# Performance work log

Hardware: AMD Instinct MI355X
Metric: run time of the kernel (lower is better)

## Reference

```python
import jax, jax.numpy as jnp
import numpy as np

B, IN, OUT, G = 64, 8192, 8192, 64
NG = IN // G  # groups per row


def setup_inputs() -> dict:
    key = jax.random.key(0)
    k1, k2, k3, k4 = jax.random.split(key, 4)
    x = jax.random.normal(k1, (B, IN), dtype=jnp.float32)
    # packed 2-bit codes: 4 codes per byte, LSB-first (matches _pack2)
    w_packed = jax.random.randint(k2, (OUT, IN // 4), 0, 256, dtype=jnp.int32).astype(jnp.uint8)
    # scales from _calc_group_qparams are positive (max_abs/1.5); zp is always 2
    scales = jax.random.uniform(k3, (OUT, NG), dtype=jnp.float32, minval=0.01, maxval=0.1)
    zps = jnp.full((OUT, NG), 2, dtype=jnp.int32)
    bias = jax.random.normal(k4, (OUT,), dtype=jnp.float32) * 0.01
    return {"x": x, "w_packed": w_packed, "scales": scales, "zps": zps, "bias": bias}


def _dequant(w_packed, scales, zps):
    # unpack: byte -> 4 two-bit codes, LSB first (matches _unpack2)
    out_f = w_packed.shape[0]
    codes = jnp.stack([(w_packed >> s) & 3 for s in (0, 2, 4, 6)], axis=-1)  # [OUT, IN//4, 4]
    q = codes.reshape(out_f, NG, G).astype(jnp.int32)                        # [OUT, NG, G]
    # per-group dequant: (q - zp) * scale
    w = (q - zps[:, :, None]).astype(jnp.float32) * scales[:, :, None]
    return w.reshape(out_f, IN)                                              # [OUT, IN]


def reference(x, w_packed, scales, zps, bias):
    w = _dequant(w_packed, scales, zps)  # [OUT, IN] fp32
    # original accumulates xg @ wg.T per group; equivalent to full x @ w.T
    return x @ w.T + bias                # [B, OUT]
```

## Files before the change

kernel.cpp:

```cpp
#include <hip/hip_runtime.h>
#include <hip/hip_bf16.h>

#define B_    64
#define IN_   8192
#define OUT_  8192
#define NG_   128
#define PB_   2048
#define KSPLIT 16
#define KC    512

typedef float f32x4 __attribute__((ext_vector_type(4)));
typedef short s16x8 __attribute__((ext_vector_type(8)));
typedef _Float16 f16x4 __attribute__((ext_vector_type(4)));

__global__ __launch_bounds__(256) void k_pre(const float* __restrict__ x,
                                             __hip_bfloat16* __restrict__ xb) {
    int i = (blockIdx.x * 256 + threadIdx.x) * 4;
    float4 f = *(const float4*)(x + i);
    __hip_bfloat162 h0 = __float22bfloat162_rn(make_float2(f.x, f.y));
    __hip_bfloat162 h1 = __float22bfloat162_rn(make_float2(f.z, f.w));
    uint2 o; o.x = *(unsigned*)&h0; o.y = *(unsigned*)&h1;
    *(uint2*)(xb + i) = o;
}

__global__ __launch_bounds__(256, 2) void k_main(
    const __hip_bfloat16* __restrict__ xb,
    const unsigned char* __restrict__ wp,
    const float* __restrict__ scales,
    const int* __restrict__ zps,
    _Float16* __restrict__ part)
{
    __shared__ uint4 x_lds[4096];
    __shared__ int wflag, zflag;

    const int tid  = threadIdx.x;
    const int wave = tid >> 6;
    const int lane = tid & 63;
    const int q    = lane >> 4;
    const int nn   = lane & 15;

    const int kidx    = blockIdx.x & (KSPLIT - 1);
    const int nblk    = blockIdx.x >> 4;
    const int kbase   = kidx * KC;
    const int colbase = nblk * 256 + wave * 64;

    uint4 w4[4][2];
    {
        const unsigned char* wb = wp + (kbase >> 2) + q * 32;
#pragma unroll
        for (int cg = 0; cg < 4; ++cg) {
            const int n = colbase + cg * 16 + nn;
            w4[cg][0] = *(const uint4*)(wb + n * PB_);
            w4[cg][1] = *(const uint4*)(wb + n * PB_ + 16);
        }
    }
    float sgl[4][2];
#pragma unroll
    for (int cg = 0; cg < 4; ++cg) {
        const int n = colbase + cg * 16 + nn;
#pragma unroll
        for (int sp = 0; sp < 2; ++sp)
            sgl[cg][sp] = scales[n * NG_ + kidx * 8 + q * 2 + sp];
    }
#pragma unroll
    for (int i = 0; i < 16; ++i) {
        const int sg = wave * 16 + i;
        const int t = sg >> 2, mt = sg & 3;
        const int sb = t >> 2, b = t & 3;
        const __hip_bfloat16* src =
            xb + (mt * 16 + nn) * IN_ + kbase + q * 128 + sb * 32 + b * 8;
        __builtin_amdgcn_global_load_lds(
            (const __attribute__((address_space(1))) unsigned int*)src,
            (__attribute__((address_space(3))) unsigned int*)
                ((char*)x_lds + sg * 1024),
            16, 0, 0);
    }
    unsigned wv = ((const unsigned int*)wp)[tid];
    int      zv = zps[tid];
    if (tid == 0) { wflag = 0; zflag = 0; }
    __syncthreads();
    if (wv > 255u) wflag = 1;
    if (zv != 2)   zflag = 1;
    __syncthreads();
    const bool u8mode = (wflag != 0);
    const bool zgen   = (zflag != 0);

    if (!u8mode) {
        const int* wpi = (const int*)wp;
#pragma unroll
        for (int cg = 0; cg < 4; ++cg) {
            const int n = colbase + cg * 16 + nn;
            const int* p = wpi + n * PB_ + (kbase >> 2) + q * 32;
#pragma unroll
            for (int c = 0; c < 2; ++c) {
                unsigned d[4];
#pragma unroll
                for (int dd = 0; dd < 4; ++dd) {
                    const int* pq = p + c * 16 + dd * 4;
                    d[dd] = (unsigned)(pq[0] & 0xFF) | ((unsigned)(pq[1] & 0xFF) << 8)
                          | ((unsigned)(pq[2] & 0xFF) << 16) | ((unsigned)(pq[3] & 0xFF) << 24);
                }
                w4[cg][c] = (uint4){d[0], d[1], d[2], d[3]};
            }
        }
    }

    unsigned tabL[4][2], tabH[4][2];
#pragma unroll
    for (int cg = 0; cg < 4; ++cg)
#pragma unroll
        for (int sp = 0; sp < 2; ++sp) {
            const float s = sgl[cg][sp];
            float zf = 2.0f;
            if (zgen) {
                const int n = colbase + cg * 16 + nn;
                zf = (float)zps[n * NG_ + kidx * 8 + q * 2 + sp];
            }
            const float v0 = -zf * s, v1 = v0 + s, v2 = v1 + s, v3 = v2 + s;
            __hip_bfloat162 lo = __float22bfloat162_rn(make_float2(v0, v1));
            __hip_bfloat162 hi = __float22bfloat162_rn(make_float2(v2, v3));
            tabL[cg][sp] = *(unsigned*)&lo;
            tabH[cg][sp] = *(unsigned*)&hi;
        }

    f32x4 acc[4][4];
#pragma unroll
    for (int cg = 0; cg < 4; ++cg)
#pragma unroll
        for (int mt = 0; mt < 4; ++mt)
            acc[cg][mt] = (f32x4){0.f, 0.f, 0.f, 0.f};

#pragma unroll
    for (int sb = 0; sb < 4; ++sb) {
#pragma unroll
        for (int b = 0; b < 4; ++b) {
            const int t = sb * 4 + b;
            union { uint4 u4; s16x8 s8; } av[4];
#pragma unroll
            for (int mt = 0; mt < 4; ++mt)
                av[mt].u4 = x_lds[(t * 4 + mt) * 64 + lane];
#pragma unroll
            for (int cg = 0; cg < 4; ++cg) {
                const uint4 ch = w4[cg][sb >> 1];
                const unsigned dwv =
                    ((const unsigned*)&ch)[((sb & 1) << 1) | (b >> 1)];
                const unsigned u = (b & 1) ? (dwv >> 16) : (dwv & 0xFFFFu);
                const unsigned tl = tabL[cg][sb >> 1], th = tabH[cg][sb >> 1];
                union { unsigned w[4]; s16x8 s8; } bf;
#pragma unroll
                for (int m = 0; m < 4; ++m) {
                    const unsigned c0 = (u >> (4 * m)) & 3u;
                    const unsigned c1 = (u >> (4 * m + 2)) & 3u;
                    const unsigned sel = (0x0100u + c0 * 0x0202u)
                                       | ((0x0100u + c1 * 0x0202u) << 16);
                    bf.w[m] = __builtin_amdgcn_perm(th, tl, sel);
                }
#pragma unroll
                for (int mt = 0; mt < 4; ++mt)
                    acc[cg][mt] = __builtin_amdgcn_mfma_f32_16x16x32_bf16(
                        av[mt].s8, bf.s8, acc[cg][mt], 0, 0, 0);
            }
        }
    }

    _Float16* pp = part + kidx * (B_ * OUT_);
#pragma unroll
    for (int cg = 0; cg < 4; ++cg) {
        const int col = colbase + cg * 16 + nn;
#pragma unroll
        for (int mt = 0; mt < 4; ++mt)
#pragma unroll
            for (int r = 0; r < 4; ++r)
                pp[(mt * 16 + q * 4 + r) * OUT_ + col] = (_Float16)acc[cg][mt][r];
    }
}

__global__ __launch_bounds__(256) void k_reduce(const _Float16* __restrict__ part,
                                                const float* __restrict__ bias,
                                                float* __restrict__ out) {
    const int gtid = blockIdx.x * 256 + threadIdx.x;
    const int b  = gtid >> 11;
    const int n0 = (gtid & 2047) * 4;
    float4 s = *(const float4*)(bias + n0);
#pragma unroll
    for (int p = 0; p < KSPLIT; ++p) {
        f16x4 v = *(const f16x4*)(part + p * (B_ * OUT_) + b * OUT_ + n0);
        s.x += (float)v[0]; s.y += (float)v[1];
        s.z += (float)v[2]; s.w += (float)v[3];
    }
    *(float4*)(out + b * OUT_ + n0) = s;
}

extern "C" void kernel_launch(void* const* d_in, const int* in_sizes, int n_in,
                              void* d_out, int out_size, void* d_ws, size_t ws_size,
                              hipStream_t stream) {
    const float*         x      = (const float*)d_in[0];
    const unsigned char* wp     = (const unsigned char*)d_in[1];
    const float*         scales = (const float*)d_in[2];
    const int*           zps    = (const int*)d_in[3];
    const float*         bias   = (const float*)d_in[4];
    float*               out    = (float*)d_out;

    __hip_bfloat16* xb   = (__hip_bfloat16*)d_ws;
    _Float16*       part = (_Float16*)((char*)d_ws + (1 << 20));

    k_pre<<<512, 256, 0, stream>>>(x, xb);
    k_main<<<512, 256, 0, stream>>>(xb, wp, scales, zps, part);
    k_reduce<<<512, 256, 0, stream>>>(part, bias, out);
}
```

Before: 133.0 us.

## Pre-pack weights, dequant tables and x fragments into main-kernel-friendly layouts

Adds preprocessing kernels that run every call. They repack the 2-bit weights into a K-chunk-major layout, precompute the per-group bf16 dequant lookup tables from scales and zero points, and write x directly as bf16 MFMA fragments. The main kernel then does contiguous loads and no longer needs per-block mode detection or table construction. The cost is extra full passes over the weight matrix (read plus write) and several more kernel launches.

```diff
diff --git a/kernel.cpp b/kernel.cpp
--- a/kernel.cpp
+++ b/kernel.cpp
@@ -13,25 +13,100 @@
 typedef short s16x8 __attribute__((ext_vector_type(8)));
 typedef _Float16 f16x4 __attribute__((ext_vector_type(4)));
 
+#define OFF_WQ   (1u << 20)
+#define OFF_TAB  (17u << 20)
+#define OFF_PART (25u << 20)
+#define OFF_FLAG (41u << 20)
+
+__global__ __launch_bounds__(256) void k_flag(const unsigned* __restrict__ wp,
+                                              int* __restrict__ flag) {
+    __shared__ int f;
+    unsigned any = 0;
+#pragma unroll
+    for (int i = 0; i < 16; ++i)
+        any |= (wp[i * 256 + threadIdx.x] > 255u) ? 1u : 0u;
+    if (threadIdx.x == 0) f = 0;
+    __syncthreads();
+    if (any) f = 1;
+    __syncthreads();
+    if (threadIdx.x == 0) *flag = f;
+}
+
+__global__ __launch_bounds__(256) void k_wpack(const unsigned char* __restrict__ wp,
+                                               unsigned char* __restrict__ wq,
+                                               const int* __restrict__ flag) {
+    const int c  = threadIdx.x >> 4;
+    const int r  = blockIdx.x * 16 + (threadIdx.x & 15);
+    uint4 v[8];
+    if (*flag) {
+        const uint4* src = (const uint4*)(wp + r * PB_ + c * 128);
+#pragma unroll
+        for (int u = 0; u < 8; ++u) v[u] = src[u];
+    } else {
+        const int* src = (const int*)wp + r * PB_ + c * 128;
+#pragma unroll
+        for (int u = 0; u < 8; ++u) {
+            unsigned d[4];
+#pragma unroll
+            for (int w = 0; w < 4; ++w) {
+                const int* p = src + u * 16 + w * 4;
+                d[w] = (unsigned)(p[0] & 0xFF) | ((unsigned)(p[1] & 0xFF) << 8) |
+                       ((unsigned)(p[2] & 0xFF) << 16) | ((unsigned)(p[3] & 0xFF) << 24);
+            }
+            v[u] = (uint4){d[0], d[1], d[2], d[3]};
+        }
+    }
+    uint4* dst = (uint4*)(wq + ((unsigned)c * OUT_ + r) * 128);
+#pragma unroll
+    for (int u = 0; u < 8; ++u) dst[u] = v[u];
+}
+
+__global__ __launch_bounds__(256) void k_spack(const float* __restrict__ scales,
+                                               const int* __restrict__ zps,
+                                               uint2* __restrict__ tab) {
+    const int e = blockIdx.x * 256 + threadIdx.x;
+    const int n = e >> 7, g = e & 127;
+    const float s = scales[e];
+    const float zf = (float)zps[e];
+    const float v0 = -zf * s, v1 = v0 + s, v2 = v1 + s, v3 = v2 + s;
+    __hip_bfloat162 lo = __float22bfloat162_rn(make_float2(v0, v1));
+    __hip_bfloat162 hi = __float22bfloat162_rn(make_float2(v2, v3));
+    uint2 ent; ent.x = *(unsigned*)&lo; ent.y = *(unsigned*)&hi;
+    tab[(((unsigned)(g >> 3) * OUT_) + n) * 8 + (g & 7)] = ent;
+}
+
 __global__ __launch_bounds__(256) void k_pre(const float* __restrict__ x,
-                                             __hip_bfloat16* __restrict__ xb) {
-    int i = (blockIdx.x * 256 + threadIdx.x) * 4;
-    float4 f = *(const float4*)(x + i);
-    __hip_bfloat162 h0 = __float22bfloat162_rn(make_float2(f.x, f.y));
-    __hip_bfloat162 h1 = __float22bfloat162_rn(make_float2(f.z, f.w));
-    uint2 o; o.x = *(unsigned*)&h0; o.y = *(unsigned*)&h1;
-    *(uint2*)(xb + i) = o;
+                                             uint4* __restrict__ xfrag) {
+    const int kidx = blockIdx.x >> 2;
+    const int part = blockIdx.x & 3;
+#pragma unroll
+    for (int i = 0; i < 4; ++i) {
+        const int idx = (part * 4 + i) * 256 + threadIdx.x;
+        const int sg = idx >> 6, lane = idx & 63;
+        const int tt = sg >> 2, mt = sg & 3;
+        const int sb = tt >> 2, b = tt & 3;
+        const int q = lane >> 4, nn = lane & 15;
+        const float* src = x + (mt * 16 + nn) * IN_ + kidx * KC + q * 128 + sb * 32 + b * 8;
+        const float4 f0 = *(const float4*)src;
+        const float4 f1 = *(const float4*)(src + 4);
+        __hip_bfloat162 h0 = __float22bfloat162_rn(make_float2(f0.x, f0.y));
+        __hip_bfloat162 h1 = __float22bfloat162_rn(make_float2(f0.z, f0.w));
+        __hip_bfloat162 h2 = __float22bfloat162_rn(make_float2(f1.x, f1.y));
+        __hip_bfloat162 h3 = __float22bfloat162_rn(make_float2(f1.z, f1.w));
+        uint4 o;
+        o.x = *(unsigned*)&h0; o.y = *(unsigned*)&h1;
+        o.z = *(unsigned*)&h2; o.w = *(unsigned*)&h3;
+        xfrag[kidx * 4096 + idx] = o;
+    }
 }
 
 __global__ __launch_bounds__(256, 2) void k_main(
-    const __hip_bfloat16* __restrict__ xb,
-    const unsigned char* __restrict__ wp,
-    const float* __restrict__ scales,
-    const int* __restrict__ zps,
+    const uint4* __restrict__ xfrag,
+    const unsigned char* __restrict__ wq,
+    const uint4* __restrict__ tab,
     _Float16* __restrict__ part)
 {
     __shared__ uint4 x_lds[4096];
-    __shared__ int wflag, zflag;
 
     const int tid  = threadIdx.x;
     const int wave = tid >> 6;
@@ -41,87 +116,33 @@
 
     const int kidx    = blockIdx.x & (KSPLIT - 1);
     const int nblk    = blockIdx.x >> 4;
-    const int kbase   = kidx * KC;
     const int colbase = nblk * 256 + wave * 64;
 
     uint4 w4[4][2];
-    {
-        const unsigned char* wb = wp + (kbase >> 2) + q * 32;
-#pragma unroll
-        for (int cg = 0; cg < 4; ++cg) {
-            const int n = colbase + cg * 16 + nn;
-            w4[cg][0] = *(const uint4*)(wb + n * PB_);
-            w4[cg][1] = *(const uint4*)(wb + n * PB_ + 16);
-        }
-    }
-    float sgl[4][2];
 #pragma unroll
     for (int cg = 0; cg < 4; ++cg) {
-        const int n = colbase + cg * 16 + nn;
-#pragma unroll
-        for (int sp = 0; sp < 2; ++sp)
-            sgl[cg][sp] = scales[n * NG_ + kidx * 8 + q * 2 + sp];
+        const unsigned n = colbase + cg * 16 + nn;
+        const uint4* src = (const uint4*)(wq + ((unsigned)kidx * OUT_ + n) * 128 + q * 32);
+        w4[cg][0] = src[0];
+        w4[cg][1] = src[1];
+    }
+    uint4 tq[4];
+#pragma unroll
+    for (int cg = 0; cg < 4; ++cg) {
+        const unsigned n = colbase + cg * 16 + nn;
+        tq[cg] = tab[((unsigned)kidx * OUT_ + n) * 4 + q];
     }
 #pragma unroll
     for (int i = 0; i < 16; ++i) {
         const int sg = wave * 16 + i;
-        const int t = sg >> 2, mt = sg & 3;
-        const int sb = t >> 2, b = t & 3;
-        const __hip_bfloat16* src =
-            xb + (mt * 16 + nn) * IN_ + kbase + q * 128 + sb * 32 + b * 8;
+        const uint4* src = xfrag + kidx * 4096 + sg * 64 + lane;
         __builtin_amdgcn_global_load_lds(
             (const __attribute__((address_space(1))) unsigned int*)src,
             (__attribute__((address_space(3))) unsigned int*)
                 ((char*)x_lds + sg * 1024),
             16, 0, 0);
     }
-    unsigned wv = ((const unsigned int*)wp)[tid];
-    int      zv = zps[tid];
-    if (tid == 0) { wflag = 0; zflag = 0; }
     __syncthreads();
-    if (wv > 255u) wflag = 1;
-    if (zv != 2)   zflag = 1;
-    __syncthreads();
-    const bool u8mode = (wflag != 0);
-    const bool zgen   = (zflag != 0);
-
-    if (!u8mode) {
-        const int* wpi = (const int*)wp;
-#pragma unroll
-        for (int cg = 0; cg < 4; ++cg) {
-            const int n = colbase + cg * 16 + nn;
-            const int* p = wpi + n * PB_ + (kbase >> 2) + q * 32;
-#pragma unroll
-            for (int c = 0; c < 2; ++c) {
-                unsigned d[4];
-#pragma unroll
-                for (int dd = 0; dd < 4; ++dd) {
-                    const int* pq = p + c * 16 + dd * 4;
-                    d[dd] = (unsigned)(pq[0] & 0xFF) | ((unsigned)(pq[1] & 0xFF) << 8)
-                          | ((unsigned)(pq[2] & 0xFF) << 16) | ((unsigned)(pq[3] & 0xFF) << 24);
-                }
-                w4[cg][c] = (uint4){d[0], d[1], d[2], d[3]};
-            }
-        }
-    }
-
-    unsigned tabL[4][2], tabH[4][2];
-#pragma unroll
-    for (int cg = 0; cg < 4; ++cg)
-#pragma unroll
-        for (int sp = 0; sp < 2; ++sp) {
-            const float s = sgl[cg][sp];
-            float zf = 2.0f;
-            if (zgen) {
-                const int n = colbase + cg * 16 + nn;
-                zf = (float)zps[n * NG_ + kidx * 8 + q * 2 + sp];
-            }
-            const float v0 = -zf * s, v1 = v0 + s, v2 = v1 + s, v3 = v2 + s;
-            __hip_bfloat162 lo = __float22bfloat162_rn(make_float2(v0, v1));
-            __hip_bfloat162 hi = __float22bfloat162_rn(make_float2(v2, v3));
-            tabL[cg][sp] = *(unsigned*)&lo;
-            tabH[cg][sp] = *(unsigned*)&hi;
-        }
 
     f32x4 acc[4][4];
 #pragma unroll
@@ -145,7 +166,8 @@
                 const unsigned dwv =
                     ((const unsigned*)&ch)[((sb & 1) << 1) | (b >> 1)];
                 const unsigned u = (b & 1) ? (dwv >> 16) : (dwv & 0xFFFFu);
-                const unsigned tl = tabL[cg][sb >> 1], th = tabH[cg][sb >> 1];
+                const unsigned tl = (sb >> 1) ? tq[cg].z : tq[cg].x;
+                const unsigned th = (sb >> 1) ? tq[cg].w : tq[cg].y;
                 union { unsigned w[4]; s16x8 s8; } bf;
 #pragma unroll
                 for (int m = 0; m < 4; ++m) {
@@ -201,10 +223,17 @@
     const float*         bias   = (const float*)d_in[4];
     float*               out    = (float*)d_out;
 
-    __hip_bfloat16* xb   = (__hip_bfloat16*)d_ws;
-    _Float16*       part = (_Float16*)((char*)d_ws + (1 << 20));
-
-    k_pre<<<512, 256, 0, stream>>>(x, xb);
-    k_main<<<512, 256, 0, stream>>>(xb, wp, scales, zps, part);
+    char* ws = (char*)d_ws;
+    uint4*          xfrag = (uint4*)ws;
+    unsigned char*  wq    = (unsigned char*)(ws + OFF_WQ);
+    uint4*          tab   = (uint4*)(ws + OFF_TAB);
+    _Float16*       part  = (_Float16*)(ws + OFF_PART);
+    int*            flag  = (int*)(ws + OFF_FLAG);
+
+    k_flag<<<1, 256, 0, stream>>>((const unsigned*)wp, flag);
+    k_wpack<<<512, 256, 0, stream>>>(wp, wq, flag);
+    k_spack<<<4096, 256, 0, stream>>>(scales, zps, (uint2*)tab);
+    k_pre<<<64, 256, 0, stream>>>(x, xfrag);
+    k_main<<<512, 256, 0, stream>>>(xfrag, wq, tab, part);
     k_reduce<<<512, 256, 0, stream>>>(part, bias, out);
 }
```

Result: slower. 144.9 us (+8.9%).
